# Kernel tuning notes

Hardware: AMD Instinct MI355X
Metric: run time of the kernel (lower is better)

Reference implementation:

```python
import jax, jax.numpy as jnp
import numpy as np

B, CH_IN, H, W = 2048, 1, 28, 28
C1, C2, C3, C4 = 16, 20, 24, 30
NODE, OUT_DIM, SP = 36, 10, 2
N = 16 * 16  # spatial nodes after 4 VALID 4x4 convs: 28->25->22->19->16
EPS = 1e-5


def _conv(x, w, b):
    # x: [B,C,H,W], w: [O,I,4,4] (torch OIHW), VALID padding
    y = jax.lax.conv_general_dilated(x, w, (1, 1), 'VALID',
                                     dimension_numbers=('NCHW', 'OIHW', 'NCHW'))
    return y + b[None, :, None, None]


def _layernorm2d(x, gamma=None, beta=None):
    # normalize jointly over last two dims (torch LayerNorm([N, node_size]))
    mu = jnp.mean(x, axis=(-2, -1), keepdims=True)
    var = jnp.mean(jnp.square(x - mu), axis=(-2, -1), keepdims=True)
    y = (x - mu) * jax.lax.rsqrt(var + EPS)
    if gamma is not None:
        y = y * gamma + beta
    return y


def setup_inputs() -> dict:
    key = jax.random.key(0)
    ks = jax.random.split(key, 32)
    d = {}
    d['x'] = jax.random.normal(ks[0], (B, CH_IN, H, W), dtype=jnp.float32)

    def init_w(k, shape, fan_in):
        return jax.random.normal(k, shape, dtype=jnp.float32) * (1.0 / np.sqrt(fan_in))

    # conv stack
    d['w1'] = init_w(ks[1], (C1, CH_IN, 4, 4), CH_IN * 16)
    d['b1'] = jnp.zeros((C1,), jnp.float32)
    d['w2'] = init_w(ks[2], (C2, C1, 4, 4), C1 * 16)
    d['b2'] = jnp.zeros((C2,), jnp.float32)
    d['w3'] = init_w(ks[3], (C3, C2, 4, 4), C2 * 16)
    d['b3'] = jnp.zeros((C3,), jnp.float32)
    d['w4'] = init_w(ks[4], (C4, C3, 4, 4), C3 * 16)
    d['b4'] = jnp.zeros((C4,), jnp.float32)

    feat = C4 + SP  # 32
    d['kW'] = init_w(ks[5], (NODE, feat), feat)
    d['kb'] = jnp.zeros((NODE,), jnp.float32)
    d['qW'] = init_w(ks[6], (NODE, feat), feat)
    d['qb'] = jnp.zeros((NODE,), jnp.float32)
    d['vW'] = init_w(ks[7], (NODE, feat), feat)
    d['vb'] = jnp.zeros((NODE,), jnp.float32)

    # affine LayerNorms over (N, node_size)
    d['kg'] = jnp.ones((N, NODE), jnp.float32)
    d['kbeta'] = jnp.zeros((N, NODE), jnp.float32)
    d['qg'] = jnp.ones((N, NODE), jnp.float32)
    d['qbeta'] = jnp.zeros((N, NODE), jnp.float32)
    d['vg'] = jnp.ones((N, NODE), jnp.float32)
    d['vbeta'] = jnp.zeros((N, NODE), jnp.float32)

    d['l1W'] = init_w(ks[8], (NODE, NODE), NODE)
    d['l1b'] = jnp.zeros((NODE,), jnp.float32)
    d['l2W'] = init_w(ks[9], (OUT_DIM, NODE), NODE)
    d['l2b'] = jnp.zeros((OUT_DIM,), jnp.float32)
    return d


def _forward(x, w1, b1, w2, b2, w3, b3, w4, b4,
             kW, kb, qW, qb, vW, vb,
             kg, kbeta, qg, qbeta, vg, vbeta,
             l1W, l1b, l2W, l2b):
    b = x.shape[0]
    # conv feature extractor with ReLU between layers
    h = jax.nn.relu(_conv(x, w1, b1))
    h = jax.nn.relu(_conv(h, w2, b2))
    h = jax.nn.relu(_conv(h, w3, b3))
    h = jax.nn.relu(_conv(h, w4, b4))  # [B, C4, 16, 16]
    ch, cw = h.shape[2], h.shape[3]

    # normalized spatial coordinate channels
    xcoords = jnp.broadcast_to(jnp.arange(cw, dtype=jnp.float32)[None, :] / cw, (ch, cw))
    ycoords = jnp.broadcast_to(jnp.arange(ch, dtype=jnp.float32)[:, None] / ch, (ch, cw))
    coords = jnp.broadcast_to(jnp.stack([xcoords, ycoords], axis=0)[None], (b, SP, ch, cw))
    h = jnp.concatenate([h, coords], axis=1)          # [B, C4+2, 16, 16]
    h = h.transpose(0, 2, 3, 1).reshape(b, ch * cw, -1)  # [B, N, 32]

    key_ = _layernorm2d(h @ kW.T + kb, kg, kbeta)     # [B, N, node]
    qry = _layernorm2d(h @ qW.T + qb, qg, qbeta)
    val = _layernorm2d(h @ vW.T + vb, vg, vbeta)

    adj = jnp.einsum('bfe,bge->bfg', qry, key_) / np.sqrt(NODE)
    adj = jax.nn.softmax(adj, axis=2)                 # [B, N, N]
    att = jnp.einsum('bfc,bcd->bfd', adj, val)        # [B, N, node]

    att = jax.nn.relu(att @ l1W.T + l1b)
    att = _layernorm2d(att)                           # no affine
    att = jnp.max(att, axis=1)                        # [B, node]
    y = att @ l2W.T + l2b
    return jax.nn.log_softmax(y, axis=1)              # [B, out_dim]


def reference(x, w1, b1, w2, b2, w3, b3, w4, b4,
              kW, kb, qW, qb, vW, vb,
              kg, kbeta, qg, qbeta, vg, vbeta,
              l1W, l1b, l2W, l2b):
    return _forward(x, w1, b1, w2, b2, w3, b3, w4, b4,
                    kW, kb, qW, qb, vW, vb,
                    kg, kbeta, qg, qbeta, vg, vbeta,
                    l1W, l1b, l2W, l2b)
```

## Files before the change

### kernel.cpp

```cpp
#include <hip/hip_runtime.h>
#include <math.h>

#define LN_EPS 1e-5f

typedef _Float16 half_t;
typedef _Float16 half8_t __attribute__((ext_vector_type(8)));
typedef _Float16 half4_t __attribute__((ext_vector_type(4)));
typedef _Float16 half2_t __attribute__((ext_vector_type(2)));
typedef float f32x4 __attribute__((ext_vector_type(4)));

__global__ void prep_weights_kernel(const float* __restrict__ w2,
                                    const float* __restrict__ w3,
                                    const float* __restrict__ w4,
                                    half_t* __restrict__ F2,
                                    half_t* __restrict__ F3,
                                    half_t* __restrict__ F4)
{
    const int bid = blockIdx.x;
    const int t   = threadIdx.x;
    const int flat0 = t * 2;
    const int l  = flat0 >> 3;
    const int j0 = flat0 & 7;

    int layer, sn;
    half_t* dst;
    if (bid < 16)      { layer = 2; sn = bid;      dst = F2; }
    else if (bid < 40) { layer = 3; sn = bid - 16; dst = F3; }
    else               { layer = 4; sn = bid - 40; dst = F4; }
    const int s  = sn >> 1;
    const int nt = sn & 1;
    const int oc = nt * 16 + (l & 15);

    float v[2];
    #pragma unroll
    for (int u = 0; u < 2; ++u) {
        const int j = j0 + u;
        const int k = s * 32 + ((l >> 4) * 8) + j;
        float val = 0.f;
        if (layer == 2) {
            const int ky = k >> 6, rem = k & 63, kx = rem >> 4, ic = rem & 15;
            if (oc < 20) val = w2[(oc * 16 + ic) * 16 + ky * 4 + kx];
        } else if (layer == 3) {
            const int ky = k / 96, rem = k % 96, kx = rem / 24, ic = rem % 24;
            if (oc < 24 && ic < 20) val = w3[(oc * 20 + ic) * 16 + ky * 4 + kx];
        } else {
            const int ky = k / 96, rem = k % 96, kx = rem / 24, ic = rem % 24;
            if (oc < 30) val = w4[(oc * 24 + ic) * 16 + ky * 4 + kx];
        }
        v[u] = val;
    }
    half2_t outv;
    outv[0] = (half_t)v[0];
    outv[1] = (half_t)v[1];
    *(half2_t*)&dst[(sn * 64 + l) * 8 + j0] = outv;
}

__global__ __launch_bounds__(256, 2) void conv_fused_kernel(
    const float* __restrict__ x,
    const float* __restrict__ w1, const float* __restrict__ b1,
    const float* __restrict__ b2, const float* __restrict__ b3,
    const float* __restrict__ b4,
    const half_t* __restrict__ F2, const half_t* __restrict__ F3,
    const half_t* __restrict__ F4,
    half_t* __restrict__ hout)
{
    __shared__ __attribute__((aligned(16))) char LBUF[45280];
    float*  xw = (float*)LBUF;
    char*   plane2b = LBUF;
    char*   plane1b = LBUF + 23232;
    half_t* plane2h = (half_t*)plane2b;
    half_t* plane1h = (half_t*)plane1b;
    half_t* plane3h = (half_t*)plane1b;
    half_t* stage   = (half_t*)plane2b;

    const int b    = blockIdx.x;
    const int tid  = threadIdx.x;
    const int wave = tid >> 6;
    const int l    = tid & 63;
    const int col  = l & 15;
    const int g    = l >> 4;

    {
        const float4* gx = (const float4*)(x + (size_t)b * 784);
        if (tid < 196) ((float4*)xw)[tid] = gx[tid];
        const int i = tid;
        if (i < 256) xw[784 + (i & 15) * 16 + (i >> 4)] = w1[i];
        if (tid < 16) xw[1040 + tid] = b1[tid];
    }
    __syncthreads();

    {
        const float* xs  = xw;
        const float* w1s = xw + 784;
        const float* b1s = xw + 1040;
        const int p0 = tid, p1 = tid + 256;
        const bool v2 = (tid + 512) < 625;
        const int p2 = v2 ? tid + 512 : 624;
        const int y0 = p0 / 25, x0 = p0 % 25;
        const int y1 = p1 / 25, x1 = p1 % 25;
        const int y2 = p2 / 25, x2 = p2 % 25;
        float a0[16], a1[16], a2[16];
        #pragma unroll
        for (int oc = 0; oc < 16; ++oc) { const float bb = b1s[oc]; a0[oc] = bb; a1[oc] = bb; a2[oc] = bb; }
        #pragma unroll
        for (int k = 0; k < 16; ++k) {
            const int ky = k >> 2, kx = k & 3;
            const float i0 = xs[(y0 + ky) * 28 + x0 + kx];
            const float i1 = xs[(y1 + ky) * 28 + x1 + kx];
            const float i2 = xs[(y2 + ky) * 28 + x2 + kx];
            #pragma unroll
            for (int oc4 = 0; oc4 < 4; ++oc4) {
                const float4 wv = *(const float4*)&w1s[k * 16 + oc4 * 4];
                const float wq[4] = {wv.x, wv.y, wv.z, wv.w};
                #pragma unroll
                for (int q = 0; q < 4; ++q) {
                    const int oc = oc4 * 4 + q;
                    a0[oc] += i0 * wq[q]; a1[oc] += i1 * wq[q]; a2[oc] += i2 * wq[q];
                }
            }
        }
        __syncthreads();
        #pragma unroll
        for (int i2_ = 0; i2_ < 8; ++i2_) {
            half2_t h0, h1;
            h0[0] = (half_t)fmaxf(a0[2 * i2_], 0.f); h0[1] = (half_t)fmaxf(a0[2 * i2_ + 1], 0.f);
            h1[0] = (half_t)fmaxf(a1[2 * i2_], 0.f); h1[1] = (half_t)fmaxf(a1[2 * i2_ + 1], 0.f);
            *(half2_t*)&plane1h[p0 * 16 + 2 * i2_] = h0;
            *(half2_t*)&plane1h[p1 * 16 + 2 * i2_] = h1;
        }
        if (v2) {
            #pragma unroll
            for (int i2_ = 0; i2_ < 8; ++i2_) {
                half2_t h2v;
                h2v[0] = (half_t)fmaxf(a2[2 * i2_], 0.f); h2v[1] = (half_t)fmaxf(a2[2 * i2_ + 1], 0.f);
                *(half2_t*)&plane1h[p2 * 16 + 2 * i2_] = h2v;
            }
        }
    }
    __syncthreads();

    {
        half8_t B2f[8][2];
        const half8_t* Fv = (const half8_t*)F2;
        #pragma unroll
        for (int s = 0; s < 8; ++s) {
            B2f[s][0] = Fv[(s * 2 + 0) * 64 + l];
            B2f[s][1] = Fv[(s * 2 + 1) * 64 + l];
        }
        const float bias0 = b2[col];
        const float bias1 = (16 + col < 20) ? b2[16 + col] : 0.f;
        #pragma unroll 1
        for (int mt = wave; mt < 31; mt += 4) {
            const int pos = mt * 16 + col;
            const int py = pos / 22, px = pos - py * 22;
            const char* Ab = plane1b + (py * 25 + px) * 32 + g * 16;
            f32x4 c0 = {0.f, 0.f, 0.f, 0.f}, c1 = {0.f, 0.f, 0.f, 0.f};
            #pragma unroll
            for (int s = 0; s < 8; ++s) {
                const half8_t a = *(const half8_t*)(Ab + (s >> 1) * 800 + (s & 1) * 64);
                c0 = __builtin_amdgcn_mfma_f32_16x16x32_f16(a, B2f[s][0], c0, 0, 0, 0);
                c1 = __builtin_amdgcn_mfma_f32_16x16x32_f16(a, B2f[s][1], c1, 0, 0, 0);
            }
            #pragma unroll
            for (int r = 0; r < 4; ++r) {
                const int prow = mt * 16 + g * 4 + r;
                if (prow < 484) {
                    plane2h[prow * 24 + col] = (half_t)fmaxf(c0[r] + bias0, 0.f);
                    if (col < 8) {
                        const float v = (col < 4) ? fmaxf(c1[r] + bias1, 0.f) : 0.f;
                        plane2h[prow * 24 + 16 + col] = (half_t)v;
                    }
                }
            }
        }
    }
    __syncthreads();

    {
        half8_t B3f[12][2];
        const half8_t* Fv = (const half8_t*)F3;
        #pragma unroll
        for (int s = 0; s < 12; ++s) {
            B3f[s][0] = Fv[(s * 2 + 0) * 64 + l];
            B3f[s][1] = Fv[(s * 2 + 1) * 64 + l];
        }
        const float bias0 = b3[col];
        const float bias1 = b3[16 + (col & 7)];
        #pragma unroll 1
        for (int mt = wave; mt < 23; mt += 4) {
            const int pos = mt * 16 + col;
            const int py = pos / 19, px = pos - py * 19;
            const char* Ab = plane2b + (py * 22 + px) * 48 + g * 16;
            f32x4 c0 = {0.f, 0.f, 0.f, 0.f}, c1 = {0.f, 0.f, 0.f, 0.f};
            #pragma unroll
            for (int s = 0; s < 12; ++s) {
                const half8_t a = *(const half8_t*)(Ab + (s / 3) * 1056 + (s % 3) * 64);
                c0 = __builtin_amdgcn_mfma_f32_16x16x32_f16(a, B3f[s][0], c0, 0, 0, 0);
                c1 = __builtin_amdgcn_mfma_f32_16x16x32_f16(a, B3f[s][1], c1, 0, 0, 0);
            }
            #pragma unroll
            for (int r = 0; r < 4; ++r) {
                const int prow = mt * 16 + g * 4 + r;
                if (prow < 361) {
                    plane3h[prow * 24 + col] = (half_t)fmaxf(c0[r] + bias0, 0.f);
                    if (col < 8)
                        plane3h[prow * 24 + 16 + col] = (half_t)fmaxf(c1[r] + bias1, 0.f);
                }
            }
        }
    }
    __syncthreads();

    {
        half8_t B4f[12][2];
        const half8_t* Fv = (const half8_t*)F4;
        #pragma unroll
        for (int s = 0; s < 12; ++s) {
            B4f[s][0] = Fv[(s * 2 + 0) * 64 + l];
            B4f[s][1] = Fv[(s * 2 + 1) * 64 + l];
        }
        const float bias0 = b4[col];
        const float bias1 = (16 + col < 30) ? b4[16 + col] : 0.f;
        #pragma unroll 1
        for (int mt = wave; mt < 16; mt += 4) {
            const int pos = mt * 16 + col;
            const int py = pos >> 4, px = pos & 15;
            const char* Ab = plane1b + (py * 19 + px) * 48 + g * 16;
            f32x4 c0 = {0.f, 0.f, 0.f, 0.f}, c1 = {0.f, 0.f, 0.f, 0.f};
            #pragma unroll
            for (int s = 0; s < 12; ++s) {
                const half8_t a = *(const half8_t*)(Ab + (s / 3) * 912 + (s % 3) * 64);
                c0 = __builtin_amdgcn_mfma_f32_16x16x32_f16(a, B4f[s][0], c0, 0, 0, 0);
                c1 = __builtin_amdgcn_mfma_f32_16x16x32_f16(a, B4f[s][1], c1, 0, 0, 0);
            }
            #pragma unroll
            for (int r = 0; r < 4; ++r) {
                const int prow = mt * 16 + g * 4 + r;
                stage[prow * 32 + col] = (half_t)fmaxf(c0[r] + bias0, 0.f);
                if (col < 14)
                    stage[prow * 32 + 16 + col] = (half_t)fmaxf(c1[r] + bias1, 0.f);
            }
        }
        half2_t cc;
        cc[0] = (half_t)((float)(tid & 15) * 0.0625f);
        cc[1] = (half_t)((float)(tid >> 4) * 0.0625f);
        *(half2_t*)&stage[tid * 32 + 30] = cc;
    }
    __syncthreads();

    {
        const float4* sst  = (const float4*)stage;
        float4* gdst = (float4*)(hout + (size_t)b * 8192);
        #pragma unroll
        for (int k2 = 0; k2 < 4; ++k2)
            gdst[tid + 256 * k2] = sst[tid + 256 * k2];
    }
}

__device__ __forceinline__ void block_reduce2(float& s1, float& s2, float* red)
{
    #pragma unroll
    for (int off = 32; off > 0; off >>= 1) {
        s1 += __shfl_down(s1, off);
        s2 += __shfl_down(s2, off);
    }
    const int lane = threadIdx.x & 63;
    const int wid  = threadIdx.x >> 6;
    if (lane == 0) { red[wid * 2] = s1; red[wid * 2 + 1] = s2; }
    __syncthreads();
    s1 = red[0] + red[2] + red[4] + red[6];
    s2 = red[1] + red[3] + red[5] + red[7];
    __syncthreads();
}

__global__ __launch_bounds__(256, 2) void attn_head_kernel(
    const half_t* __restrict__ hbuf,
    const float* __restrict__ kW, const float* __restrict__ kb,
    const float* __restrict__ qW, const float* __restrict__ qb,
    const float* __restrict__ vW, const float* __restrict__ vb,
    const float* __restrict__ kg, const float* __restrict__ kbeta,
    const float* __restrict__ qg, const float* __restrict__ qbeta,
    const float* __restrict__ vg, const float* __restrict__ vbeta,
    const float* __restrict__ l1W, const float* __restrict__ l1b,
    const float* __restrict__ l2W, const float* __restrict__ l2b,
    float* __restrict__ out)
{
    __shared__ __attribute__((aligned(16))) char LDS[73728];
    __shared__ float red[8];
    __shared__ float epi[196];

    half_t* Qbuf = (half_t*)LDS;
    half_t* Kbuf = (half_t*)(LDS + 24576);
    half_t* Vt   = (half_t*)(LDS + 49152);
    float*  mbuf = (float*)(LDS + 24576);

    const int b   = blockIdx.x;
    const int tid = threadIdx.x;
    const int w   = tid >> 6;
    const int l   = tid & 63;
    const int c   = l & 15;
    const int g   = l >> 4;

    half8_t hA[4];
    #pragma unroll
    for (int mt = 0; mt < 4; ++mt)
        hA[mt] = *(const half8_t*)(hbuf + ((size_t)b * 256 + 64 * w + 16 * mt + c) * 32 + 8 * g);

    #pragma unroll 1
    for (int pj = 0; pj < 3; ++pj) {
        const float* W    = (pj == 0) ? kW : (pj == 1) ? vW : qW;
        const float* bias = (pj == 0) ? kb : (pj == 1) ? vb : qb;
        const float* gam  = (pj == 0) ? kg : (pj == 1) ? vg : qg;
        const float* bet  = (pj == 0) ? kbeta : (pj == 1) ? vbeta : qbeta;

        half8_t Bf[3];
        #pragma unroll
        for (int nt = 0; nt < 3; ++nt) {
            const int row = 16 * nt + c;
            half8_t hb;
            if (row < 36) {
                const float4 w0 = *(const float4*)(W + row * 32 + 8 * g);
                const float4 w1 = *(const float4*)(W + row * 32 + 8 * g + 4);
                hb[0] = (half_t)w0.x; hb[1] = (half_t)w0.y; hb[2] = (half_t)w0.z; hb[3] = (half_t)w0.w;
                hb[4] = (half_t)w1.x; hb[5] = (half_t)w1.y; hb[6] = (half_t)w1.z; hb[7] = (half_t)w1.w;
            } else {
                #pragma unroll
                for (int j = 0; j < 8; ++j) hb[j] = (half_t)0.f;
            }
            Bf[nt] = hb;
        }
        f32x4 acc[4][3];
        #pragma unroll
        for (int nt = 0; nt < 3; ++nt) {
            const int o = 16 * nt + c;
            const float bv = (o < 36) ? bias[o] : 0.f;
            #pragma unroll
            for (int mt = 0; mt < 4; ++mt) acc[mt][nt] = (f32x4){bv, bv, bv, bv};
        }
        #pragma unroll
        for (int mt = 0; mt < 4; ++mt)
            #pragma unroll
            for (int nt = 0; nt < 3; ++nt)
                acc[mt][nt] = __builtin_amdgcn_mfma_f32_16x16x32_f16(hA[mt], Bf[nt], acc[mt][nt], 0, 0, 0);

        #pragma unroll
        for (int mt = 0; mt < 4; ++mt)
            #pragma unroll
            for (int nt = 0; nt < 3; ++nt)
                #pragma unroll
                for (int r = 0; r < 4; ++r)
                    Qbuf[(64 * w + 16 * mt + 4 * g + r) * 48 + 16 * nt + c] = (half_t)acc[mt][nt][r];
        __syncthreads();

        float rv[36];
        {
            const half_t* rp = Qbuf + tid * 48;
            #pragma unroll
            for (int j = 0; j < 36; ++j) rv[j] = (float)rp[j];
        }
        float s1 = 0.f, s2 = 0.f;
        #pragma unroll
        for (int j = 0; j < 36; ++j) { s1 += rv[j]; s2 += rv[j] * rv[j]; }
        block_reduce2(s1, s2, red);
        const float mu  = s1 * (1.0f / 9216.0f);
        const float var = s2 * (1.0f / 9216.0f) - mu * mu;
        const float rs  = rsqrtf(var + LN_EPS);

        half_t rowb[48];
        #pragma unroll
        for (int j4 = 0; j4 < 9; ++j4) {
            const float4 gm = *(const float4*)(gam + tid * 36 + 4 * j4);
            const float4 bt = *(const float4*)(bet + tid * 36 + 4 * j4);
            float f0 = (rv[4*j4+0] - mu) * rs * gm.x + bt.x;
            float f1 = (rv[4*j4+1] - mu) * rs * gm.y + bt.y;
            float f2 = (rv[4*j4+2] - mu) * rs * gm.z + bt.z;
            float f3 = (rv[4*j4+3] - mu) * rs * gm.w + bt.w;
            if (pj == 2) { f0 *= (1.0f/6.0f); f1 *= (1.0f/6.0f); f2 *= (1.0f/6.0f); f3 *= (1.0f/6.0f); }
            rowb[4*j4+0] = (half_t)f0; rowb[4*j4+1] = (half_t)f1;
            rowb[4*j4+2] = (half_t)f2; rowb[4*j4+3] = (half_t)f3;
        }
        #pragma unroll
        for (int j = 36; j < 48; ++j) rowb[j] = (half_t)0.f;

        if (pj == 0) {
            #pragma unroll
            for (int i = 0; i < 6; ++i)
                *(half8_t*)(Kbuf + tid * 48 + 8 * i) = *(half8_t*)&rowb[8 * i];
        } else if (pj == 1) {
            #pragma unroll
            for (int j = 0; j < 36; ++j)
                Vt[j * 256 + (tid ^ ((j & 7) << 2))] = rowb[j];
        } else {
            #pragma unroll
            for (int i = 0; i < 6; ++i)
                *(half8_t*)(Qbuf + tid * 48 + 8 * i) = *(half8_t*)&rowb[8 * i];
        }
        __syncthreads();
    }

    half8_t Qf32[4];
    half4_t Qf16[4];
    #pragma unroll
    for (int nt = 0; nt < 4; ++nt) {
        const int row = 64 * w + 16 * nt + c;
        Qf32[nt] = *(const half8_t*)(Qbuf + row * 48 + 8 * g);
        Qf16[nt] = *(const half4_t*)(Qbuf + row * 48 + 32 + 4 * g);
    }

    float m[4], lsum[4];
    f32x4 att[3][4];
    #pragma unroll
    for (int nt = 0; nt < 4; ++nt) {
        m[nt] = -1e30f; lsum[nt] = 0.f;
        #pragma unroll
        for (int mt2 = 0; mt2 < 3; ++mt2) att[mt2][nt] = (f32x4){0.f, 0.f, 0.f, 0.f};
    }

    #pragma unroll 1
    for (int ch = 0; ch < 8; ++ch) {
        half8_t Ka32[2];
        half4_t Ka16[2];
        #pragma unroll
        for (int mt = 0; mt < 2; ++mt) {
            const int row = 32 * ch + 16 * mt + c;
            Ka32[mt] = *(const half8_t*)(Kbuf + row * 48 + 8 * g);
            Ka16[mt] = *(const half4_t*)(Kbuf + row * 48 + 32 + 4 * g);
        }
        half4_t Va[3][2];
        #pragma unroll
        for (int mt2 = 0; mt2 < 3; ++mt2)
            #pragma unroll
            for (int kc = 0; kc < 2; ++kc)
                Va[mt2][kc] = *(const half4_t*)(Vt + (16 * mt2 + c) * 256 +
                                ((32 * ch + 16 * kc + 4 * g) ^ ((c & 7) << 2)));

        f32x4 S[2][4];
        #pragma unroll
        for (int mt = 0; mt < 2; ++mt)
            #pragma unroll
            for (int nt = 0; nt < 4; ++nt) {
                f32x4 z = {0.f, 0.f, 0.f, 0.f};
                z = __builtin_amdgcn_mfma_f32_16x16x32_f16(Ka32[mt], Qf32[nt], z, 0, 0, 0);
                z = __builtin_amdgcn_mfma_f32_16x16x16f16(Ka16[mt], Qf16[nt], z, 0, 0, 0);
                S[mt][nt] = z;
            }

        #pragma unroll
        for (int nt = 0; nt < 4; ++nt) {
            float cm = S[0][nt][0];
            cm = fmaxf(cm, S[0][nt][1]); cm = fmaxf(cm, S[0][nt][2]); cm = fmaxf(cm, S[0][nt][3]);
            cm = fmaxf(cm, S[1][nt][0]); cm = fmaxf(cm, S[1][nt][1]);
            cm = fmaxf(cm, S[1][nt][2]); cm = fmaxf(cm, S[1][nt][3]);
            cm = fmaxf(cm, __shfl_xor(cm, 16));
            cm = fmaxf(cm, __shfl_xor(cm, 32));
            const float newm  = fmaxf(m[nt], cm);
            const float alpha = __expf(m[nt] - newm);
            m[nt] = newm;
            lsum[nt] *= alpha;
            #pragma unroll
            for (int mt2 = 0; mt2 < 3; ++mt2) att[mt2][nt] *= alpha;

            half4_t P[2];
            #pragma unroll
            for (int mt = 0; mt < 2; ++mt) {
                const float p0 = __expf(S[mt][nt][0] - newm);
                const float p1 = __expf(S[mt][nt][1] - newm);
                const float p2 = __expf(S[mt][nt][2] - newm);
                const float p3 = __expf(S[mt][nt][3] - newm);
                lsum[nt] += (p0 + p1) + (p2 + p3);
                half4_t pp;
                pp[0] = (half_t)p0; pp[1] = (half_t)p1; pp[2] = (half_t)p2; pp[3] = (half_t)p3;
                P[mt] = pp;
            }
            #pragma unroll
            for (int mt2 = 0; mt2 < 3; ++mt2) {
                att[mt2][nt] = __builtin_amdgcn_mfma_f32_16x16x16f16(Va[mt2][0], P[0], att[mt2][nt], 0, 0, 0);
                att[mt2][nt] = __builtin_amdgcn_mfma_f32_16x16x16f16(Va[mt2][1], P[1], att[mt2][nt], 0, 0, 0);
            }
        }
    }

    #pragma unroll
    for (int nt = 0; nt < 4; ++nt) {
        float lt = lsum[nt];
        lt += __shfl_xor(lt, 16);
        lt += __shfl_xor(lt, 32);
        const float inv = 1.0f / lt;
        const int row = 64 * w + 16 * nt + c;
        #pragma unroll
        for (int mt2 = 0; mt2 < 2; ++mt2)
            #pragma unroll
            for (int r = 0; r < 4; ++r)
                Qbuf[row * 48 + 16 * mt2 + 4 * g + r] = (half_t)(att[mt2][nt][r] * inv);
        if (g == 0) {
            #pragma unroll
            for (int r = 0; r < 4; ++r)
                Qbuf[row * 48 + 32 + r] = (half_t)(att[2][nt][r] * inv);
        }
    }
    __syncthreads();

    float at[36];
    #pragma unroll
    for (int j = 0; j < 36; ++j) at[j] = (float)Qbuf[tid * 48 + j];

    float a2[36];
    #pragma unroll
    for (int jj = 0; jj < 36; ++jj) {
        float s = l1b[jj];
        #pragma unroll
        for (int d = 0; d < 36; ++d) s += at[d] * l1W[jj * 36 + d];
        a2[jj] = fmaxf(s, 0.f);
    }

    float s1 = 0.f, s2 = 0.f;
    #pragma unroll
    for (int j = 0; j < 36; ++j) { s1 += a2[j]; s2 += a2[j] * a2[j]; }
    block_reduce2(s1, s2, red);
    const float mu  = s1 * (1.0f / 9216.0f);
    const float rs  = rsqrtf(s2 * (1.0f / 9216.0f) - mu * mu + LN_EPS);

    float a3[36];
    #pragma unroll
    for (int j = 0; j < 36; ++j) a3[j] = (a2[j] - mu) * rs;

    #pragma unroll
    for (int off = 1; off < 64; off <<= 1)
        #pragma unroll
        for (int j = 0; j < 36; ++j)
            a3[j] = fmaxf(a3[j], __shfl_xor(a3[j], off));
    if (l == 0) {
        #pragma unroll
        for (int j = 0; j < 36; ++j) epi[w * 36 + j] = a3[j];
    }
    __syncthreads();
    if (tid < 36)
        epi[144 + tid] = fmaxf(fmaxf(epi[tid], epi[36 + tid]),
                               fmaxf(epi[72 + tid], epi[108 + tid]));
    __syncthreads();
    if (tid < 10) {
        float y = l2b[tid];
        #pragma unroll
        for (int j = 0; j < 36; ++j) y += epi[144 + j] * l2W[tid * 36 + j];
        epi[180 + tid] = y;
    }
    __syncthreads();
    if (tid == 0) {
        float mx = epi[180];
        #pragma unroll
        for (int cc = 1; cc < 10; ++cc) mx = fmaxf(mx, epi[180 + cc]);
        float se = 0.f;
        #pragma unroll
        for (int cc = 0; cc < 10; ++cc) se += __expf(epi[180 + cc] - mx);
        const float lse = mx + logf(se);
        #pragma unroll
        for (int cc = 0; cc < 10; ++cc) out[b * 10 + cc] = epi[180 + cc] - lse;
    }
}

extern "C" void kernel_launch(void* const* d_in, const int* in_sizes, int n_in,
                              void* d_out, int out_size, void* d_ws, size_t ws_size,
                              hipStream_t stream)
{
    const float* x     = (const float*)d_in[0];
    const float* w1    = (const float*)d_in[1];
    const float* b1    = (const float*)d_in[2];
    const float* w2    = (const float*)d_in[3];
    const float* b2    = (const float*)d_in[4];
    const float* w3    = (const float*)d_in[5];
    const float* b3    = (const float*)d_in[6];
    const float* w4    = (const float*)d_in[7];
    const float* b4    = (const float*)d_in[8];
    const float* kW    = (const float*)d_in[9];
    const float* kb    = (const float*)d_in[10];
    const float* qW    = (const float*)d_in[11];
    const float* qb    = (const float*)d_in[12];
    const float* vW    = (const float*)d_in[13];
    const float* vb    = (const float*)d_in[14];
    const float* kg    = (const float*)d_in[15];
    const float* kbeta = (const float*)d_in[16];
    const float* qg    = (const float*)d_in[17];
    const float* qbeta = (const float*)d_in[18];
    const float* vg    = (const float*)d_in[19];
    const float* vbeta = (const float*)d_in[20];
    const float* l1W   = (const float*)d_in[21];
    const float* l1b   = (const float*)d_in[22];
    const float* l2W   = (const float*)d_in[23];
    const float* l2b   = (const float*)d_in[24];

    const int B = in_sizes[0] / (28 * 28);
    half_t* hbuf = (half_t*)d_ws;
    half_t* F2 = (half_t*)((char*)d_ws + 33554432);
    half_t* F3 = F2 + 8192;
    half_t* F4 = F3 + 12288;

    prep_weights_kernel<<<dim3(64), dim3(256), 0, stream>>>(w2, w3, w4, F2, F3, F4);
    conv_fused_kernel<<<dim3(B), dim3(256), 0, stream>>>(
        x, w1, b1, b2, b3, b4, F2, F3, F4, hbuf);
    attn_head_kernel<<<dim3(B), dim3(256), 0, stream>>>(
        hbuf, kW, kb, qW, qb, vW, vb,
        kg, kbeta, qg, qbeta, vg, vbeta,
        l1W, l1b, l2W, l2b, (float*)d_out);
}
```

Before: 277.7 us.

## Shrink attention LDS to 48KB by reordering Q/V/K projections and raise occupancy

```diff
diff --git a/kernel.cpp b/kernel.cpp
--- a/kernel.cpp
+++ b/kernel.cpp
@@ -273,7 +273,81 @@
     __syncthreads();
 }
 
-__global__ __launch_bounds__(256, 2) void attn_head_kernel(
+__device__ __forceinline__ void proj_scatter(const half8_t hA[4],
+                                             const float* __restrict__ W,
+                                             const float* __restrict__ bias,
+                                             half_t* scr, int w, int c, int g)
+{
+    half8_t Bf[3];
+    #pragma unroll
+    for (int nt = 0; nt < 3; ++nt) {
+        const int row = 16 * nt + c;
+        half8_t hb;
+        if (row < 36) {
+            const float4 w0 = *(const float4*)(W + row * 32 + 8 * g);
+            const float4 w1 = *(const float4*)(W + row * 32 + 8 * g + 4);
+            hb[0] = (half_t)w0.x; hb[1] = (half_t)w0.y; hb[2] = (half_t)w0.z; hb[3] = (half_t)w0.w;
+            hb[4] = (half_t)w1.x; hb[5] = (half_t)w1.y; hb[6] = (half_t)w1.z; hb[7] = (half_t)w1.w;
+        } else {
+            #pragma unroll
+            for (int j = 0; j < 8; ++j) hb[j] = (half_t)0.f;
+        }
+        Bf[nt] = hb;
+    }
+    f32x4 acc[4][3];
+    #pragma unroll
+    for (int nt = 0; nt < 3; ++nt) {
+        const int o = 16 * nt + c;
+        const float bv = (o < 36) ? bias[o] : 0.f;
+        #pragma unroll
+        for (int mt = 0; mt < 4; ++mt) acc[mt][nt] = (f32x4){bv, bv, bv, bv};
+    }
+    #pragma unroll
+    for (int mt = 0; mt < 4; ++mt)
+        #pragma unroll
+        for (int nt = 0; nt < 3; ++nt)
+            acc[mt][nt] = __builtin_amdgcn_mfma_f32_16x16x32_f16(hA[mt], Bf[nt], acc[mt][nt], 0, 0, 0);
+    #pragma unroll
+    for (int mt = 0; mt < 4; ++mt)
+        #pragma unroll
+        for (int nt = 0; nt < 3; ++nt)
+            #pragma unroll
+            for (int r = 0; r < 4; ++r)
+                scr[(64 * w + 16 * mt + 4 * g + r) * 48 + 16 * nt + c] = (half_t)acc[mt][nt][r];
+}
+
+__device__ __forceinline__ void ln_row(const half_t* buf, int tid,
+                                       const float* __restrict__ gam,
+                                       const float* __restrict__ bet,
+                                       float scale, float* red, half_t* rowb)
+{
+    float rv[36];
+    {
+        const half_t* rp = buf + tid * 48;
+        #pragma unroll
+        for (int j = 0; j < 36; ++j) rv[j] = (float)rp[j];
+    }
+    float s1 = 0.f, s2 = 0.f;
+    #pragma unroll
+    for (int j = 0; j < 36; ++j) { s1 += rv[j]; s2 += rv[j] * rv[j]; }
+    block_reduce2(s1, s2, red);
+    const float mu  = s1 * (1.0f / 9216.0f);
+    const float var = s2 * (1.0f / 9216.0f) - mu * mu;
+    const float rs  = rsqrtf(var + LN_EPS);
+    #pragma unroll
+    for (int j4 = 0; j4 < 9; ++j4) {
+        const float4 gm = *(const float4*)(gam + tid * 36 + 4 * j4);
+        const float4 bt = *(const float4*)(bet + tid * 36 + 4 * j4);
+        rowb[4*j4+0] = (half_t)(((rv[4*j4+0] - mu) * rs * gm.x + bt.x) * scale);
+        rowb[4*j4+1] = (half_t)(((rv[4*j4+1] - mu) * rs * gm.y + bt.y) * scale);
+        rowb[4*j4+2] = (half_t)(((rv[4*j4+2] - mu) * rs * gm.z + bt.z) * scale);
+        rowb[4*j4+3] = (half_t)(((rv[4*j4+3] - mu) * rs * gm.w + bt.w) * scale);
+    }
+    #pragma unroll
+    for (int j = 36; j < 48; ++j) rowb[j] = (half_t)0.f;
+}
+
+__global__ __launch_bounds__(256, 3) void attn_head_kernel(
     const half_t* __restrict__ hbuf,
     const float* __restrict__ kW, const float* __restrict__ kb,
     const float* __restrict__ qW, const float* __restrict__ qb,
@@ -285,14 +359,13 @@
     const float* __restrict__ l2W, const float* __restrict__ l2b,
     float* __restrict__ out)
 {
-    __shared__ __attribute__((aligned(16))) char LDS[73728];
+    __shared__ __attribute__((aligned(16))) char LDS[49152];
     __shared__ float red[8];
     __shared__ float epi[196];
 
-    half_t* Qbuf = (half_t*)LDS;
-    half_t* Kbuf = (half_t*)(LDS + 24576);
-    half_t* Vt   = (half_t*)(LDS + 49152);
-    float*  mbuf = (float*)(LDS + 24576);
+    half_t* BufA = (half_t*)LDS;
+    half_t* BufB = (half_t*)(LDS + 24576);
+    half_t* Vt   = (half_t*)(LDS + 24576);
 
     const int b   = blockIdx.x;
     const int tid = threadIdx.x;
@@ -306,106 +379,48 @@
     for (int mt = 0; mt < 4; ++mt)
         hA[mt] = *(const half8_t*)(hbuf + ((size_t)b * 256 + 64 * w + 16 * mt + c) * 32 + 8 * g);
 
-    #pragma unroll 1
-    for (int pj = 0; pj < 3; ++pj) {
-        const float* W    = (pj == 0) ? kW : (pj == 1) ? vW : qW;
-        const float* bias = (pj == 0) ? kb : (pj == 1) ? vb : qb;
-        const float* gam  = (pj == 0) ? kg : (pj == 1) ? vg : qg;
-        const float* bet  = (pj == 0) ? kbeta : (pj == 1) ? vbeta : qbeta;
-
-        half8_t Bf[3];
-        #pragma unroll
-        for (int nt = 0; nt < 3; ++nt) {
-            const int row = 16 * nt + c;
-            half8_t hb;
-            if (row < 36) {
-                const float4 w0 = *(const float4*)(W + row * 32 + 8 * g);
-                const float4 w1 = *(const float4*)(W + row * 32 + 8 * g + 4);
-                hb[0] = (half_t)w0.x; hb[1] = (half_t)w0.y; hb[2] = (half_t)w0.z; hb[3] = (half_t)w0.w;
-                hb[4] = (half_t)w1.x; hb[5] = (half_t)w1.y; hb[6] = (half_t)w1.z; hb[7] = (half_t)w1.w;
-            } else {
-                #pragma unroll
-                for (int j = 0; j < 8; ++j) hb[j] = (half_t)0.f;
-            }
-            Bf[nt] = hb;
-        }
-        f32x4 acc[4][3];
-        #pragma unroll
-        for (int nt = 0; nt < 3; ++nt) {
-            const int o = 16 * nt + c;
-            const float bv = (o < 36) ? bias[o] : 0.f;
-            #pragma unroll
-            for (int mt = 0; mt < 4; ++mt) acc[mt][nt] = (f32x4){bv, bv, bv, bv};
-        }
-        #pragma unroll
-        for (int mt = 0; mt < 4; ++mt)
-            #pragma unroll
-            for (int nt = 0; nt < 3; ++nt)
-                acc[mt][nt] = __builtin_amdgcn_mfma_f32_16x16x32_f16(hA[mt], Bf[nt], acc[mt][nt], 0, 0, 0);
-
-        #pragma unroll
-        for (int mt = 0; mt < 4; ++mt)
-            #pragma unroll
-            for (int nt = 0; nt < 3; ++nt)
-                #pragma unroll
-                for (int r = 0; r < 4; ++r)
-                    Qbuf[(64 * w + 16 * mt + 4 * g + r) * 48 + 16 * nt + c] = (half_t)acc[mt][nt][r];
-        __syncthreads();
-
-        float rv[36];
-        {
-            const half_t* rp = Qbuf + tid * 48;
-            #pragma unroll
-            for (int j = 0; j < 36; ++j) rv[j] = (float)rp[j];
-        }
-        float s1 = 0.f, s2 = 0.f;
-        #pragma unroll
-        for (int j = 0; j < 36; ++j) { s1 += rv[j]; s2 += rv[j] * rv[j]; }
-        block_reduce2(s1, s2, red);
-        const float mu  = s1 * (1.0f / 9216.0f);
-        const float var = s2 * (1.0f / 9216.0f) - mu * mu;
-        const float rs  = rsqrtf(var + LN_EPS);
-
+    proj_scatter(hA, qW, qb, BufA, w, c, g);
+    proj_scatter(hA, vW, vb, BufB, w, c, g);
+    __syncthreads();
+
+    {
         half_t rowb[48];
-        #pragma unroll
-        for (int j4 = 0; j4 < 9; ++j4) {
-            const float4 gm = *(const float4*)(gam + tid * 36 + 4 * j4);
-            const float4 bt = *(const float4*)(bet + tid * 36 + 4 * j4);
-            float f0 = (rv[4*j4+0] - mu) * rs * gm.x + bt.x;
-            float f1 = (rv[4*j4+1] - mu) * rs * gm.y + bt.y;
-            float f2 = (rv[4*j4+2] - mu) * rs * gm.z + bt.z;
-            float f3 = (rv[4*j4+3] - mu) * rs * gm.w + bt.w;
-            if (pj == 2) { f0 *= (1.0f/6.0f); f1 *= (1.0f/6.0f); f2 *= (1.0f/6.0f); f3 *= (1.0f/6.0f); }
-            rowb[4*j4+0] = (half_t)f0; rowb[4*j4+1] = (half_t)f1;
-            rowb[4*j4+2] = (half_t)f2; rowb[4*j4+3] = (half_t)f3;
-        }
-        #pragma unroll
-        for (int j = 36; j < 48; ++j) rowb[j] = (half_t)0.f;
-
-        if (pj == 0) {
-            #pragma unroll
-            for (int i = 0; i < 6; ++i)
-                *(half8_t*)(Kbuf + tid * 48 + 8 * i) = *(half8_t*)&rowb[8 * i];
-        } else if (pj == 1) {
-            #pragma unroll
-            for (int j = 0; j < 36; ++j)
-                Vt[j * 256 + (tid ^ ((j & 7) << 2))] = rowb[j];
-        } else {
-            #pragma unroll
-            for (int i = 0; i < 6; ++i)
-                *(half8_t*)(Qbuf + tid * 48 + 8 * i) = *(half8_t*)&rowb[8 * i];
-        }
-        __syncthreads();
-    }
+        ln_row(BufA, tid, qg, qbeta, (1.0f / 6.0f), red, rowb);
+        #pragma unroll
+        for (int i = 0; i < 6; ++i)
+            *(half8_t*)(BufA + tid * 48 + 8 * i) = *(half8_t*)&rowb[8 * i];
+    }
+    {
+        half_t rowb[48];
+        ln_row(BufB, tid, vg, vbeta, 1.0f, red, rowb);
+        #pragma unroll
+        for (int j = 0; j < 48; ++j) {
+            const half_t v = (j < 36) ? rowb[j] : (half_t)0.f;
+            Vt[j * 256 + (tid ^ ((j & 7) << 2))] = v;
+        }
+    }
+    __syncthreads();
 
     half8_t Qf32[4];
     half4_t Qf16[4];
     #pragma unroll
     for (int nt = 0; nt < 4; ++nt) {
         const int row = 64 * w + 16 * nt + c;
-        Qf32[nt] = *(const half8_t*)(Qbuf + row * 48 + 8 * g);
-        Qf16[nt] = *(const half4_t*)(Qbuf + row * 48 + 32 + 4 * g);
-    }
+        Qf32[nt] = *(const half8_t*)(BufA + row * 48 + 8 * g);
+        Qf16[nt] = *(const half4_t*)(BufA + row * 48 + 32 + 4 * g);
+    }
+    __syncthreads();
+
+    proj_scatter(hA, kW, kb, BufA, w, c, g);
+    __syncthreads();
+    {
+        half_t rowb[48];
+        ln_row(BufA, tid, kg, kbeta, 1.0f, red, rowb);
+        #pragma unroll
+        for (int i = 0; i < 6; ++i)
+            *(half8_t*)(BufA + tid * 48 + 8 * i) = *(half8_t*)&rowb[8 * i];
+    }
+    __syncthreads();
 
     float m[4], lsum[4];
     f32x4 att[3][4];
@@ -421,10 +436,10 @@
         half8_t Ka32[2];
         half4_t Ka16[2];
         #pragma unroll
-        for (int mt = 0; mt < 2; ++mt) {
-            const int row = 32 * ch + 16 * mt + c;
-            Ka32[mt] = *(const half8_t*)(Kbuf + row * 48 + 8 * g);
-            Ka16[mt] = *(const half4_t*)(Kbuf + row * 48 + 32 + 4 * g);
+        for (int kt = 0; kt < 2; ++kt) {
+            const int row = 32 * ch + 16 * kt + c;
+            Ka32[kt] = *(const half8_t*)(BufA + row * 48 + 8 * g);
+            Ka16[kt] = *(const half4_t*)(BufA + row * 48 + 32 + 4 * g);
         }
         half4_t Va[3][2];
         #pragma unroll
@@ -436,13 +451,13 @@
 
         f32x4 S[2][4];
         #pragma unroll
-        for (int mt = 0; mt < 2; ++mt)
+        for (int kt = 0; kt < 2; ++kt)
             #pragma unroll
             for (int nt = 0; nt < 4; ++nt) {
                 f32x4 z = {0.f, 0.f, 0.f, 0.f};
-                z = __builtin_amdgcn_mfma_f32_16x16x32_f16(Ka32[mt], Qf32[nt], z, 0, 0, 0);
-                z = __builtin_amdgcn_mfma_f32_16x16x16f16(Ka16[mt], Qf16[nt], z, 0, 0, 0);
-                S[mt][nt] = z;
+                z = __builtin_amdgcn_mfma_f32_16x16x32_f16(Ka32[kt], Qf32[nt], z, 0, 0, 0);
+                z = __builtin_amdgcn_mfma_f32_16x16x16f16(Ka16[kt], Qf16[nt], z, 0, 0, 0);
+                S[kt][nt] = z;
             }
 
         #pragma unroll
@@ -462,15 +477,15 @@
 
             half4_t P[2];
             #pragma unroll
-            for (int mt = 0; mt < 2; ++mt) {
-                const float p0 = __expf(S[mt][nt][0] - newm);
-                const float p1 = __expf(S[mt][nt][1] - newm);
-                const float p2 = __expf(S[mt][nt][2] - newm);
-                const float p3 = __expf(S[mt][nt][3] - newm);
+            for (int kt = 0; kt < 2; ++kt) {
+                const float p0 = __expf(S[kt][nt][0] - newm);
+                const float p1 = __expf(S[kt][nt][1] - newm);
+                const float p2 = __expf(S[kt][nt][2] - newm);
+                const float p3 = __expf(S[kt][nt][3] - newm);
                 lsum[nt] += (p0 + p1) + (p2 + p3);
                 half4_t pp;
                 pp[0] = (half_t)p0; pp[1] = (half_t)p1; pp[2] = (half_t)p2; pp[3] = (half_t)p3;
-                P[mt] = pp;
+                P[kt] = pp;
             }
             #pragma unroll
             for (int mt2 = 0; mt2 < 3; ++mt2) {
@@ -479,6 +494,7 @@
             }
         }
     }
+    __syncthreads();
 
     #pragma unroll
     for (int nt = 0; nt < 4; ++nt) {
@@ -491,18 +507,21 @@
         for (int mt2 = 0; mt2 < 2; ++mt2)
             #pragma unroll
             for (int r = 0; r < 4; ++r)
-                Qbuf[row * 48 + 16 * mt2 + 4 * g + r] = (half_t)(att[mt2][nt][r] * inv);
+                BufA[row * 48 + 16 * mt2 + 4 * g + r] = (half_t)(att[mt2][nt][r] * inv);
         if (g == 0) {
             #pragma unroll
             for (int r = 0; r < 4; ++r)
-                Qbuf[row * 48 + 32 + r] = (half_t)(att[2][nt][r] * inv);
+                BufA[row * 48 + 32 + r] = (half_t)(att[2][nt][r] * inv);
         }
     }
     __syncthreads();
 
     float at[36];
-    #pragma unroll
-    for (int j = 0; j < 36; ++j) at[j] = (float)Qbuf[tid * 48 + j];
+    {
+        const half_t* rp = BufA + tid * 48;
+        #pragma unroll
+        for (int j = 0; j < 36; ++j) at[j] = (float)rp[j];
+    }
 
     float a2[36];
     #pragma unroll
```

Result: faster. 262.3 us (-5.5%).
